# Kernel optimization log

Hardware: AMD Instinct MI355X
Metric: run time of the kernel (lower is better)

The kernel has to match this reference:

```python
import jax, jax.numpy as jnp
import numpy as np

ROWS, COLS = 4096, 8192
K = 4096                      # target_mask_size (<= COLS)
TEMPERATURE = 2.0 / 3.0


def setup_inputs() -> dict:
    key = jax.random.key(0)
    k1, k2 = jax.random.split(key)
    # param_init_fn: normal(mean=log(1-0.5)-log(0.5)=0, std=0.01)
    z_loga = jax.random.normal(k1, (ROWS, COLS), dtype=jnp.float32) * 0.01
    # eps = rand_like(...).clamp_(1e-6, 1-1e-6)
    eps = jax.random.uniform(k2, (ROWS, COLS), dtype=jnp.float32,
                             minval=1e-6, maxval=1.0 - 1e-6)
    return {"z_loga": z_loga, "eps": eps, "step": 0}


def reference(z_loga, eps, step):
    # Training branch of Mask.sample_z: gumbel-sigmoid + per-row top-k hard mask
    # with straight-through estimator.
    gumbel = -jnp.log(-jnp.log(eps))                       # [R, C]
    gumbel_mask = jax.nn.sigmoid((z_loga + gumbel) / TEMPERATURE)
    # per-row top-k hard selection (dim=1), scatter ones at top-k indices
    _, idx = jax.lax.top_k(gumbel_mask, K)                 # [R, K]
    rows = jnp.arange(gumbel_mask.shape[0])[:, None]       # [R, 1]
    hard = jnp.zeros_like(gumbel_mask).at[rows, idx].set(1.0)
    # straight-through: forward = hard, gradient flows through gumbel_mask
    st = hard - jax.lax.stop_gradient(gumbel_mask) + gumbel_mask
    return st.reshape(ROWS, COLS)                          # mask_output_shape
```

## Files before the change

### kernel.cpp

```cpp
#include <hip/hip_runtime.h>
#include <math.h>
#include <stdint.h>

#define ROWS 4096
#define COLS 8192
#define KSEL 4096
#define NT 256
#define NWAVE (NT / 64)
#define PT (COLS / (4 * NT))
#define NBINS 1024
#define WMAX 128
#define RANGE_HI 0.75f
#define LN2F 0.69314718056f

__device__ __forceinline__ int bin_of(float u) {
    int b = (int)(u * ((float)NBINS / RANGE_HI));
    b = b < 0 ? 0 : b;
    b = b > NBINS - 1 ? NBINS - 1 : b;
    return b;
}

__global__ __launch_bounds__(NT) void mask_topk_kernel(
    const float* __restrict__ z, const float* __restrict__ eps,
    float* __restrict__ out)
{
    __shared__ uint32_t hist[NWAVE][NBINS];
    __shared__ uint32_t wtot[NWAVE];
    __shared__ int      winIdx[WMAX];
    __shared__ uint32_t winSig[WMAX];
    __shared__ int      s_B, s_need2;
    __shared__ uint32_t s_SB, s_wcount;

    const int row  = blockIdx.x;
    const int tid  = threadIdx.x;
    const int lane = tid & 63;
    const int wave = tid >> 6;
    const size_t rbase = (size_t)row * COLS;

    const float4* z4 = (const float4*)(z + rbase);
    const float4* e4 = (const float4*)(eps + rbase);
    float4 zr[PT], er[PT];
#pragma unroll
    for (int it = 0; it < PT; ++it) {
        zr[it] = z4[it * NT + tid];
        er[it] = e4[it * NT + tid];
    }
    __builtin_amdgcn_sched_barrier(0);

    for (int i = tid; i < NWAVE * NBINS; i += NT) ((uint32_t*)hist)[i] = 0;
    if (tid == 0) s_wcount = 0;
    __syncthreads();

#pragma unroll
    for (int it = 0; it < PT; ++it) {
        float zz[4] = {zr[it].x, zr[it].y, zr[it].z, zr[it].w};
        float ee[4] = {er[it].x, er[it].y, er[it].z, er[it].w};
        float uu[4];
#pragma unroll
        for (int j = 0; j < 4; ++j) {
            float l1 = __builtin_amdgcn_logf(ee[j]) * LN2F;
            float l2 = __builtin_amdgcn_logf(-l1) * LN2F;
            uu[j] = zz[j] - l2;
            atomicAdd(&hist[wave][bin_of(uu[j])], 1u);
        }
        zr[it].x = uu[0]; zr[it].y = uu[1]; zr[it].z = uu[2]; zr[it].w = uu[3];
    }
    __syncthreads();

    const int hb = tid * (NBINS / NT);
    uint32_t h[NBINS / NT];
    uint32_t cs = 0;
#pragma unroll
    for (int i = 0; i < NBINS / NT; ++i) {
        uint32_t t = 0;
#pragma unroll
        for (int c = 0; c < NWAVE; ++c) t += hist[c][hb + i];
        h[i] = t;
        cs += t;
    }
    uint32_t v = cs;
#pragma unroll
    for (int off = 1; off < 64; off <<= 1) {
        uint32_t t = __shfl_down(v, off, 64);
        if (lane + off < 64) v += t;
    }
    if (lane == 0) wtot[wave] = v;
    __syncthreads();
    uint32_t above = 0;
#pragma unroll
    for (int c = 0; c < NWAVE; ++c) above += (c > wave) ? wtot[c] : 0u;
    uint32_t cum = (v + above) - cs;

    for (int i = NBINS / NT - 1; i >= 0; --i) {
        if (cum < KSEL && KSEL <= cum + h[i]) { s_B = hb + i; s_SB = cum; }
        cum += h[i];
    }
    __syncthreads();
    const int B = s_B;
    if (tid == 0) {
        uint32_t hB1 = 0;
        if (B + 1 < NBINS)
            for (int c = 0; c < NWAVE; ++c) hB1 += hist[c][B + 1];
        s_need2 = KSEL - (int)(s_SB - hB1);
    }
    __syncthreads();
    const int need2 = s_need2;

    float4* o4 = (float4*)(out + rbase);
#pragma unroll
    for (int it = 0; it < PT; ++it) {
        const int k = it * NT + tid;
        float uu[4] = {zr[it].x, zr[it].y, zr[it].z, zr[it].w};
        float oo[4];
#pragma unroll
        for (int j = 0; j < 4; ++j) {
            int b = bin_of(uu[j]);
            oo[j] = (b > B + 1) ? 1.0f : 0.0f;
            if (b >= B - 1 && b <= B + 1) {
                uint32_t slot = atomicAdd(&s_wcount, 1u);
                if (slot < WMAX) winIdx[slot] = k * 4 + j;
            }
        }
        float4 ov; ov.x = oo[0]; ov.y = oo[1]; ov.z = oo[2]; ov.w = oo[3];
        o4[k] = ov;
    }
    __syncthreads();

    int w = (int)s_wcount; if (w > WMAX) w = WMAX;
    if (tid < 64) {
        for (int j = lane; j < w; j += 64) {
            int idx = winIdx[j];
            float e  = eps[rbase + idx];
            float zz = z[rbase + idx];
            float l1  = (float)log((double)e);
            float l2  = (float)log((double)(-l1));
            float g   = -l2;
            float s   = zz + g;
            float t   = s / (2.0f / 3.0f);
            float ex  = (float)exp(-(double)t);
            float sig = 1.0f / (1.0f + ex);
            winSig[j] = __float_as_uint(sig);
        }
    }
    __syncthreads();
    if (tid < 64) {
        for (int j = lane; j < w; j += 64) {
            uint32_t sj = winSig[j];
            int ij = winIdx[j];
            int rank = 0;
            for (int kk = 0; kk < w; ++kk) {
                uint32_t sk = winSig[kk];
                int ik = winIdx[kk];
                rank += (sk > sj || (sk == sj && ik < ij)) ? 1 : 0;
            }
            out[rbase + ij] = (rank < need2) ? 1.0f : 0.0f;
        }
    }
}

extern "C" void kernel_launch(void* const* d_in, const int* in_sizes, int n_in,
                              void* d_out, int out_size, void* d_ws, size_t ws_size,
                              hipStream_t stream) {
    const float* z   = (const float*)d_in[0];
    const float* eps = (const float*)d_in[1];
    float* out = (float*)d_out;
    hipLaunchKernelGGL(mask_topk_kernel, dim3(ROWS), dim3(NT), 0, stream,
                       z, eps, out);
}
```

Measured before the change: 318.9 us.

## Process two rows per block with software-pipelined loads and packed bin storage

```diff
diff --git a/kernel.cpp b/kernel.cpp
--- a/kernel.cpp
+++ b/kernel.cpp
@@ -13,6 +13,8 @@
 #define RANGE_HI 0.75f
 #define LN2F 0.69314718056f
 
+typedef float fvec4 __attribute__((ext_vector_type(4)));
+
 __device__ __forceinline__ int bin_of(float u) {
     int b = (int)(u * ((float)NBINS / RANGE_HI));
     b = b < 0 ? 0 : b;
@@ -20,7 +22,15 @@
     return b;
 }
 
-__global__ __launch_bounds__(NT) void mask_topk_kernel(
+#define LGKM_BAR() do { \
+    asm volatile("s_waitcnt lgkmcnt(0)" ::: "memory"); \
+    __builtin_amdgcn_s_barrier(); } while (0)
+
+#define FULL_BAR() do { \
+    asm volatile("s_waitcnt vmcnt(0) lgkmcnt(0)" ::: "memory"); \
+    __builtin_amdgcn_s_barrier(); } while (0)
+
+__global__ __launch_bounds__(NT, 2) void mask_topk_kernel(
     const float* __restrict__ z, const float* __restrict__ eps,
     float* __restrict__ out)
 {
@@ -31,131 +41,215 @@
     __shared__ int      s_B, s_need2;
     __shared__ uint32_t s_SB, s_wcount;
 
-    const int row  = blockIdx.x;
     const int tid  = threadIdx.x;
     const int lane = tid & 63;
     const int wave = tid >> 6;
-    const size_t rbase = (size_t)row * COLS;
-
-    const float4* z4 = (const float4*)(z + rbase);
-    const float4* e4 = (const float4*)(eps + rbase);
-    float4 zr[PT], er[PT];
-#pragma unroll
-    for (int it = 0; it < PT; ++it) {
-        zr[it] = z4[it * NT + tid];
-        er[it] = e4[it * NT + tid];
-    }
-    __builtin_amdgcn_sched_barrier(0);
+    const size_t rb0 = (size_t)(blockIdx.x * 2) * COLS;
+    const size_t rb1 = rb0 + COLS;
+
+#define ISSUE_LOADS(ZR, ER, RB) do {                                          \
+    const fvec4* z4_ = (const fvec4*)(z + (RB));                              \
+    const fvec4* e4_ = (const fvec4*)(eps + (RB));                            \
+    _Pragma("unroll")                                                         \
+    for (int it = 0; it < PT; ++it) {                                         \
+        const fvec4* zp_ = z4_ + (it * NT + tid);                             \
+        const fvec4* ep_ = e4_ + (it * NT + tid);                             \
+        asm volatile("global_load_dwordx4 %0, %1, off" : "=v"(ZR[it]) : "v"(zp_)); \
+        asm volatile("global_load_dwordx4 %0, %1, off" : "=v"(ER[it]) : "v"(ep_)); \
+    }                                                                         \
+    __builtin_amdgcn_sched_barrier(0);                                        \
+} while (0)
+
+#define CSTEP(ZR, ER, PB, IT, VMN, CLO, CHI) do {                             \
+    asm volatile("s_waitcnt vmcnt(" #VMN ")");                                \
+    __builtin_amdgcn_sched_barrier(0);                                        \
+    float zz_[4] = {ZR[IT].x, ZR[IT].y, ZR[IT].z, ZR[IT].w};                  \
+    float ee_[4] = {ER[IT].x, ER[IT].y, ER[IT].z, ER[IT].w};                  \
+    uint32_t bb_[4];                                                          \
+    _Pragma("unroll")                                                         \
+    for (int j = 0; j < 4; ++j) {                                             \
+        float l1_ = __builtin_amdgcn_logf(ee_[j]) * LN2F;                     \
+        float l2_ = __builtin_amdgcn_logf(-l1_) * LN2F;                       \
+        float u_  = zz_[j] - l2_;                                             \
+        int b_ = bin_of(u_);                                                  \
+        if (b_ == 0)              ++CLO;                                      \
+        else if (b_ == NBINS - 1) ++CHI;                                      \
+        else atomicAdd(&hist[wave][b_], 1u);                                  \
+        bb_[j] = (uint32_t)b_;                                                \
+    }                                                                         \
+    PB[2*(IT)]   = bb_[0] | (bb_[1] << 16);                                   \
+    PB[2*(IT)+1] = bb_[2] | (bb_[3] << 16);                                   \
+} while (0)
+
+#define CLAMP_REDUCE(CLO, CHI) do {                                           \
+    _Pragma("unroll")                                                         \
+    for (int off = 32; off >= 1; off >>= 1) {                                 \
+        CLO += __shfl_down(CLO, off, 64);                                     \
+        CHI += __shfl_down(CHI, off, 64);                                     \
+    }                                                                         \
+    if (lane == 0) {                                                          \
+        atomicAdd(&hist[wave][0],         CLO);                               \
+        atomicAdd(&hist[wave][NBINS - 1], CHI);                               \
+    }                                                                         \
+} while (0)
+
+#define SCAN_PICK(BOUT, NOUT) do {                                            \
+    const int hb_ = tid * (NBINS / NT);                                       \
+    uint32_t h_[NBINS / NT]; uint32_t cs_ = 0;                                \
+    _Pragma("unroll")                                                         \
+    for (int i = 0; i < NBINS / NT; ++i) {                                    \
+        uint32_t t_ = 0;                                                      \
+        _Pragma("unroll")                                                     \
+        for (int c = 0; c < NWAVE; ++c) t_ += hist[c][hb_ + i];               \
+        h_[i] = t_; cs_ += t_;                                                \
+    }                                                                         \
+    uint32_t v_ = cs_;                                                        \
+    _Pragma("unroll")                                                         \
+    for (int off = 1; off < 64; off <<= 1) {                                  \
+        uint32_t t_ = __shfl_down(v_, off, 64);                               \
+        if (lane + off < 64) v_ += t_;                                        \
+    }                                                                         \
+    if (lane == 0) wtot[wave] = v_;                                           \
+    LGKM_BAR();                                                               \
+    uint32_t above_ = 0;                                                      \
+    _Pragma("unroll")                                                         \
+    for (int c = 0; c < NWAVE; ++c) above_ += (c > wave) ? wtot[c] : 0u;      \
+    uint32_t cum_ = (v_ + above_) - cs_;                                      \
+    for (int i = NBINS / NT - 1; i >= 0; --i) {                               \
+        if (cum_ < KSEL && KSEL <= cum_ + h_[i]) { s_B = hb_ + i; s_SB = cum_; } \
+        cum_ += h_[i];                                                        \
+    }                                                                         \
+    LGKM_BAR();                                                               \
+    if (tid == 0) {                                                           \
+        uint32_t hB1_ = 0; int Bq_ = s_B;                                     \
+        if (Bq_ + 1 < NBINS)                                                  \
+            for (int c = 0; c < NWAVE; ++c) hB1_ += hist[c][Bq_ + 1];         \
+        s_need2 = KSEL - (int)(s_SB - hB1_);                                  \
+    }                                                                         \
+    LGKM_BAR();                                                               \
+    BOUT = s_B; NOUT = s_need2;                                               \
+} while (0)
+
+#define PASS2_STORE(PB, RB, BQ) do {                                          \
+    fvec4* o4_ = (fvec4*)(out + (RB));                                        \
+    _Pragma("unroll")                                                         \
+    for (int it = 0; it < PT; ++it) {                                         \
+        const int k_ = it * NT + tid;                                         \
+        int b_[4] = { (int)(PB[2*it] & 0xffffu), (int)(PB[2*it] >> 16),       \
+                      (int)(PB[2*it+1] & 0xffffu), (int)(PB[2*it+1] >> 16) }; \
+        float oo_[4];                                                         \
+        _Pragma("unroll")                                                     \
+        for (int j = 0; j < 4; ++j) {                                         \
+            oo_[j] = (b_[j] > (BQ) + 1) ? 1.0f : 0.0f;                        \
+            if (b_[j] >= (BQ) - 1 && b_[j] <= (BQ) + 1) {                     \
+                uint32_t slot_ = atomicAdd(&s_wcount, 1u);                    \
+                if (slot_ < WMAX) winIdx[slot_] = k_ * 4 + j;                 \
+            }                                                                 \
+        }                                                                     \
+        fvec4 ov_; ov_.x = oo_[0]; ov_.y = oo_[1]; ov_.z = oo_[2]; ov_.w = oo_[3]; \
+        o4_[k_] = ov_;                                                        \
+    }                                                                         \
+} while (0)
+
+#define TAILSIG(RB, W) do {                                                   \
+    if (tid < 64) {                                                           \
+        for (int j = lane; j < (W); j += 64) {                                \
+            int idx_ = winIdx[j];                                             \
+            float e_  = eps[(RB) + idx_];                                     \
+            float zz_ = z[(RB) + idx_];                                       \
+            float l1_ = (float)log((double)e_);                               \
+            float l2_ = (float)log((double)(-l1_));                           \
+            float g_  = -l2_;                                                 \
+            float s_  = zz_ + g_;                                             \
+            float t_  = s_ / (2.0f / 3.0f);                                   \
+            float ex_ = (float)exp(-(double)t_);                              \
+            float sig_ = 1.0f / (1.0f + ex_);                                 \
+            winSig[j] = __float_as_uint(sig_);                                \
+        }                                                                     \
+    }                                                                         \
+} while (0)
+
+#define TAILRANK(RB, W, NEED) do {                                            \
+    if (tid < 64) {                                                           \
+        for (int j = lane; j < (W); j += 64) {                                \
+            uint32_t sj_ = winSig[j]; int ij_ = winIdx[j]; int rank_ = 0;     \
+            for (int kk = 0; kk < (W); ++kk) {                                \
+                uint32_t sk_ = winSig[kk]; int ik_ = winIdx[kk];              \
+                rank_ += (sk_ > sj_ || (sk_ == sj_ && ik_ < ij_)) ? 1 : 0;    \
+            }                                                                 \
+            out[(RB) + ij_] = (rank_ < (NEED)) ? 1.0f : 0.0f;                 \
+        }                                                                     \
+    }                                                                         \
+} while (0)
+
+    fvec4 zr0[PT], er0[PT];
+    ISSUE_LOADS(zr0, er0, rb0);
 
     for (int i = tid; i < NWAVE * NBINS; i += NT) ((uint32_t*)hist)[i] = 0;
     if (tid == 0) s_wcount = 0;
-    __syncthreads();
-
-#pragma unroll
-    for (int it = 0; it < PT; ++it) {
-        float zz[4] = {zr[it].x, zr[it].y, zr[it].z, zr[it].w};
-        float ee[4] = {er[it].x, er[it].y, er[it].z, er[it].w};
-        float uu[4];
-#pragma unroll
-        for (int j = 0; j < 4; ++j) {
-            float l1 = __builtin_amdgcn_logf(ee[j]) * LN2F;
-            float l2 = __builtin_amdgcn_logf(-l1) * LN2F;
-            uu[j] = zz[j] - l2;
-            atomicAdd(&hist[wave][bin_of(uu[j])], 1u);
-        }
-        zr[it].x = uu[0]; zr[it].y = uu[1]; zr[it].z = uu[2]; zr[it].w = uu[3];
+    LGKM_BAR();
+
+    uint32_t pb0[2 * PT];
+    uint32_t cLo0 = 0, cHi0 = 0;
+    CSTEP(zr0, er0, pb0, 0, 14, cLo0, cHi0); CSTEP(zr0, er0, pb0, 1, 12, cLo0, cHi0);
+    CSTEP(zr0, er0, pb0, 2, 10, cLo0, cHi0); CSTEP(zr0, er0, pb0, 3,  8, cLo0, cHi0);
+    CSTEP(zr0, er0, pb0, 4,  6, cLo0, cHi0); CSTEP(zr0, er0, pb0, 5,  4, cLo0, cHi0);
+    CSTEP(zr0, er0, pb0, 6,  2, cLo0, cHi0); CSTEP(zr0, er0, pb0, 7,  0, cLo0, cHi0);
+    CLAMP_REDUCE(cLo0, cHi0);
+    LGKM_BAR();
+
+    fvec4 zr1[PT], er1[PT];
+    ISSUE_LOADS(zr1, er1, rb1);
+
+    int B0, need0;
+    SCAN_PICK(B0, need0);
+
+    for (int i = tid; i < NWAVE * NBINS; i += NT) ((uint32_t*)hist)[i] = 0;
+    LGKM_BAR();
+
+    uint32_t pb1[2 * PT];
+    uint32_t cLo1 = 0, cHi1 = 0;
+    CSTEP(zr1, er1, pb1, 0, 14, cLo1, cHi1); CSTEP(zr1, er1, pb1, 1, 12, cLo1, cHi1);
+    CSTEP(zr1, er1, pb1, 2, 10, cLo1, cHi1); CSTEP(zr1, er1, pb1, 3,  8, cLo1, cHi1);
+    CSTEP(zr1, er1, pb1, 4,  6, cLo1, cHi1); CSTEP(zr1, er1, pb1, 5,  4, cLo1, cHi1);
+    CSTEP(zr1, er1, pb1, 6,  2, cLo1, cHi1); CSTEP(zr1, er1, pb1, 7,  0, cLo1, cHi1);
+    CLAMP_REDUCE(cLo1, cHi1);
+    LGKM_BAR();
+
+    PASS2_STORE(pb0, rb0, B0);
+
+    int B1, need1;
+    SCAN_PICK(B1, need1);
+
+    FULL_BAR();
+
+    {
+        int w0 = (int)s_wcount; if (w0 > WMAX) w0 = WMAX;
+        TAILSIG(rb0, w0);
+        LGKM_BAR();
+        TAILRANK(rb0, w0, need0);
+        if (tid == 0) s_wcount = 0;
+        LGKM_BAR();
     }
-    __syncthreads();
-
-    const int hb = tid * (NBINS / NT);
-    uint32_t h[NBINS / NT];
-    uint32_t cs = 0;
-#pragma unroll
-    for (int i = 0; i < NBINS / NT; ++i) {
-        uint32_t t = 0;
-#pragma unroll
-        for (int c = 0; c < NWAVE; ++c) t += hist[c][hb + i];
-        h[i] = t;
-        cs += t;
+
+    PASS2_STORE(pb1, rb1, B1);
+
+    FULL_BAR();
+
+    {
+        int w1 = (int)s_wcount; if (w1 > WMAX) w1 = WMAX;
+        TAILSIG(rb1, w1);
+        LGKM_BAR();
+        TAILRANK(rb1, w1, need1);
     }
-    uint32_t v = cs;
-#pragma unroll
-    for (int off = 1; off < 64; off <<= 1) {
-        uint32_t t = __shfl_down(v, off, 64);
-        if (lane + off < 64) v += t;
-    }
-    if (lane == 0) wtot[wave] = v;
-    __syncthreads();
-    uint32_t above = 0;
-#pragma unroll
-    for (int c = 0; c < NWAVE; ++c) above += (c > wave) ? wtot[c] : 0u;
-    uint32_t cum = (v + above) - cs;
-
-    for (int i = NBINS / NT - 1; i >= 0; --i) {
-        if (cum < KSEL && KSEL <= cum + h[i]) { s_B = hb + i; s_SB = cum; }
-        cum += h[i];
-    }
-    __syncthreads();
-    const int B = s_B;
-    if (tid == 0) {
-        uint32_t hB1 = 0;
-        if (B + 1 < NBINS)
-            for (int c = 0; c < NWAVE; ++c) hB1 += hist[c][B + 1];
-        s_need2 = KSEL - (int)(s_SB - hB1);
-    }
-    __syncthreads();
-    const int need2 = s_need2;
-
-    float4* o4 = (float4*)(out + rbase);
-#pragma unroll
-    for (int it = 0; it < PT; ++it) {
-        const int k = it * NT + tid;
-        float uu[4] = {zr[it].x, zr[it].y, zr[it].z, zr[it].w};
-        float oo[4];
-#pragma unroll
-        for (int j = 0; j < 4; ++j) {
-            int b = bin_of(uu[j]);
-            oo[j] = (b > B + 1) ? 1.0f : 0.0f;
-            if (b >= B - 1 && b <= B + 1) {
-                uint32_t slot = atomicAdd(&s_wcount, 1u);
-                if (slot < WMAX) winIdx[slot] = k * 4 + j;
-            }
-        }
-        float4 ov; ov.x = oo[0]; ov.y = oo[1]; ov.z = oo[2]; ov.w = oo[3];
-        o4[k] = ov;
-    }
-    __syncthreads();
-
-    int w = (int)s_wcount; if (w > WMAX) w = WMAX;
-    if (tid < 64) {
-        for (int j = lane; j < w; j += 64) {
-            int idx = winIdx[j];
-            float e  = eps[rbase + idx];
-            float zz = z[rbase + idx];
-            float l1  = (float)log((double)e);
-            float l2  = (float)log((double)(-l1));
-            float g   = -l2;
-            float s   = zz + g;
-            float t   = s / (2.0f / 3.0f);
-            float ex  = (float)exp(-(double)t);
-            float sig = 1.0f / (1.0f + ex);
-            winSig[j] = __float_as_uint(sig);
-        }
-    }
-    __syncthreads();
-    if (tid < 64) {
-        for (int j = lane; j < w; j += 64) {
-            uint32_t sj = winSig[j];
-            int ij = winIdx[j];
-            int rank = 0;
-            for (int kk = 0; kk < w; ++kk) {
-                uint32_t sk = winSig[kk];
-                int ik = winIdx[kk];
-                rank += (sk > sj || (sk == sj && ik < ij)) ? 1 : 0;
-            }
-            out[rbase + ij] = (rank < need2) ? 1.0f : 0.0f;
-        }
-    }
+
+#undef ISSUE_LOADS
+#undef CSTEP
+#undef CLAMP_REDUCE
+#undef SCAN_PICK
+#undef PASS2_STORE
+#undef TAILSIG
+#undef TAILRANK
 }
 
 extern "C" void kernel_launch(void* const* d_in, const int* in_sizes, int n_in,
@@ -164,6 +258,6 @@
     const float* z   = (const float*)d_in[0];
     const float* eps = (const float*)d_in[1];
     float* out = (float*)d_out;
-    hipLaunchKernelGGL(mask_topk_kernel, dim3(ROWS), dim3(NT), 0, stream,
+    hipLaunchKernelGGL(mask_topk_kernel, dim3(ROWS / 2), dim3(NT), 0, stream,
                        z, eps, out);
 }
```

Result: slower. 330.2 us (+3.5%).
